# Kernel optimization log

Hardware: AMD Instinct MI355X
Metric: run time of the kernel (lower is better)

The kernel has to match this reference:

```python
import jax, jax.numpy as jnp
import numpy as np


def setup_inputs() -> dict:
    key = jax.random.key(0)
    k1, k2 = jax.random.split(key)
    B, N, M, D = 4, 8192, 8192, 3
    pred_points = jax.random.normal(k1, (B, N, D), dtype=jnp.float32)
    gt_points = jax.random.normal(k2, (B, M, D), dtype=jnp.float32)
    return {"pred_points": pred_points, "gt_points": gt_points}


def reference(pred_points, gt_points):
    p2 = jnp.sum(pred_points * pred_points, axis=-1)  # [B, N]
    g2 = jnp.sum(gt_points * gt_points, axis=-1)      # [B, M]
    cross = jnp.einsum("bnd,bmd->bnm", pred_points, gt_points)  # [B, N, M]
    d2 = p2[:, :, None] + g2[:, None, :] - 2.0 * cross
    dist = jnp.sqrt(jnp.maximum(d2, 0.0))             # [B, N, M]
    min_pred_to_gt = jnp.min(dist, axis=-1)           # [B, N]
    min_gt_to_pred = jnp.min(dist, axis=-2)           # [B, M]
    return min_pred_to_gt.mean() + min_gt_to_pred.mean()
```

## Files before the change

kernel.cpp:

```cpp
#include <hip/hip_runtime.h>


#define B_ 4
#define N_ 8192
#define TM 1024
#define SM (N_ / TM)
#define THREADS 512
#define INF32 3.4e38f

__device__ __forceinline__ float min3f(float a, float b, float c) {
  float d;
  asm("v_min3_f32 %0, %1, %2, %3" : "=v"(d) : "v"(a), "v"(b), "v"(c));
  return d;
}

__global__ __launch_bounds__(THREADS, 4) void chamfer_sym(
    const float* __restrict__ pred, const float* __restrict__ gt,
    float* __restrict__ rowpart, unsigned* __restrict__ colpart,
    float* __restrict__ accws, int RC) {
  __shared__ float4 mlds[TM];
  __shared__ unsigned colbuf[TM];

  const int b = blockIdx.z, tn = blockIdx.y, tm = blockIdx.x;
  const int tid = threadIdx.x;
  const int j = tid & 31;
  const int iq = tid >> 5;
  const int SN = gridDim.y;
  const int TN = N_ / SN;

  if (b == 0 && tn == 0 && tm == 0 && tid == 0) {
    accws[0] = 0.0f;
    ((unsigned*)accws)[1] = 0u;
  }

  const float* qsrc = pred + (size_t)b * N_ * 3;
  const float* tsrc = gt + (size_t)b * N_ * 3;

  if (tid < 256) {
    const float* tb = tsrc + (size_t)tm * TM * 3 + tid * 12;
    const float4 f0 = *(const float4*)(tb);
    const float4 f1 = *(const float4*)(tb + 4);
    const float4 f2 = *(const float4*)(tb + 8);
    float4 P0 = make_float4(f0.x, f0.y, f0.z, fmaf(f0.x,f0.x, fmaf(f0.y,f0.y, f0.z*f0.z)));
    float4 P1 = make_float4(f0.w, f1.x, f1.y, fmaf(f0.w,f0.w, fmaf(f1.x,f1.x, f1.y*f1.y)));
    float4 P2 = make_float4(f1.z, f1.w, f2.x, fmaf(f1.z,f1.z, fmaf(f1.w,f1.w, f2.x*f2.x)));
    float4 P3 = make_float4(f2.y, f2.z, f2.w, fmaf(f2.y,f2.y, fmaf(f2.z,f2.z, f2.w*f2.w)));
    const int s = (tid >> 3) & 3;
    const int base = tid * 4;
    mlds[base + (0 ^ s)] = P0;
    mlds[base + (1 ^ s)] = P1;
    mlds[base + (2 ^ s)] = P2;
    mlds[base + (3 ^ s)] = P3;
    ((uint4*)colbuf)[tid] = make_uint4(0x7F7FFFFFu, 0x7F7FFFFFu, 0x7F7FFFFFu, 0x7F7FFFFFu);
  }

  float colacc[32];
#pragma unroll
  for (int c = 0; c < 32; ++c) colacc[c] = INF32;

  __syncthreads();

  const int sw = (j >> 3) & 3;
  const int a0 = 4 * j + (0 ^ sw);
  const int a1 = 4 * j + (1 ^ sw);
  const int a2 = 4 * j + (2 ^ sw);
  const int a3 = 4 * j + (3 ^ sw);

  for (int rc = 0; rc < RC; ++rc) {
    const int r0 = tn * TN + rc * 64 + iq * 4;
    const float* qb = qsrc + (size_t)r0 * 3;
    const float4 g0 = *(const float4*)(qb);
    const float4 g1 = *(const float4*)(qb + 4);
    const float4 g2 = *(const float4*)(qb + 8);
    const float qx[4] = {g0.x, g0.w, g1.z, g2.y};
    const float qy[4] = {g0.y, g1.x, g1.w, g2.z};
    const float qz[4] = {g0.z, g1.y, g2.x, g2.w};
    float nx[4], ny[4], nz[4], q2[4], racc[4];
#pragma unroll
    for (int r = 0; r < 4; ++r) {
      nx[r] = -2.0f * qx[r]; ny[r] = -2.0f * qy[r]; nz[r] = -2.0f * qz[r];
      q2[r] = fmaf(qx[r], qx[r], fmaf(qy[r], qy[r], qz[r] * qz[r]));
      racc[r] = INF32;
    }

#pragma unroll
    for (int cs = 0; cs < 8; ++cs) {
      const float4 t0 = mlds[cs * 128 + a0];
      const float4 t1 = mlds[cs * 128 + a1];
      const float4 t2 = mlds[cs * 128 + a2];
      const float4 t3 = mlds[cs * 128 + a3];
      float sc[4][4];
#pragma unroll
      for (int r = 0; r < 4; ++r) {
        sc[r][0] = fmaf(nx[r], t0.x, fmaf(ny[r], t0.y, fmaf(nz[r], t0.z, t0.w)));
        sc[r][1] = fmaf(nx[r], t1.x, fmaf(ny[r], t1.y, fmaf(nz[r], t1.z, t1.w)));
        sc[r][2] = fmaf(nx[r], t2.x, fmaf(ny[r], t2.y, fmaf(nz[r], t2.z, t2.w)));
        sc[r][3] = fmaf(nx[r], t3.x, fmaf(ny[r], t3.y, fmaf(nz[r], t3.z, t3.w)));
        racc[r] = min3f(racc[r], sc[r][0], sc[r][1]);
        racc[r] = min3f(racc[r], sc[r][2], sc[r][3]);
      }
#pragma unroll
      for (int c = 0; c < 4; ++c) {
        colacc[cs*4+c] = min3f(colacc[cs*4+c], sc[0][c] + q2[0], sc[1][c] + q2[1]);
        colacc[cs*4+c] = min3f(colacc[cs*4+c], sc[2][c] + q2[2], sc[3][c] + q2[3]);
      }
    }

#pragma unroll
    for (int m = 1; m <= 16; m <<= 1) {
#pragma unroll
      for (int r = 0; r < 4; ++r)
        racc[r] = fminf(racc[r], __shfl_xor(racc[r], m, 64));
    }
    if (j == 0) {
      float4 v = make_float4(racc[0] + q2[0], racc[1] + q2[1],
                             racc[2] + q2[2], racc[3] + q2[3]);
      *(float4*)&rowpart[((size_t)b * SM + tm) * N_ + r0] = v;
    }
  }

#pragma unroll
  for (int c = 0; c < 32; ++c)
    colacc[c] = fminf(colacc[c], __shfl_xor(colacc[c], 32, 64));
  if ((tid & 32) == 0) {
#pragma unroll
    for (int cs = 0; cs < 8; ++cs)
#pragma unroll
      for (int c = 0; c < 4; ++c)
        atomicMin(&colbuf[cs * 128 + 4 * j + c],
                  __float_as_uint(fmaxf(colacc[cs*4+c], 0.0f)));
  }
  __syncthreads();
  {
    unsigned* dst = colpart + ((size_t)b * SN + tn) * N_ + tm * TM;
    dst[tid] = colbuf[tid];
    dst[tid + 512] = colbuf[tid + 512];
  }
}

__global__ __launch_bounds__(256) void chamfer_fin(
    const float* __restrict__ rowpart, const unsigned* __restrict__ colpart,
    float* __restrict__ accws, float* __restrict__ out, int SN) {
  const int t = blockIdx.x * 256 + threadIdx.x;
  float v;
  if (t < 32768) {
    const int b = t >> 13, n = t & (N_ - 1);
    const float* p = rowpart + (size_t)b * SM * N_ + n;
    v = p[0];
#pragma unroll
    for (int s2 = 1; s2 < SM; ++s2) v = fminf(v, p[(size_t)s2 * N_]);
  } else {
    const int u = t - 32768;
    const int b = u >> 13, n = u & (N_ - 1);
    const unsigned* p = colpart + (size_t)b * SN * N_ + n;
    unsigned m = p[0];
    for (int s2 = 1; s2 < SN; ++s2) m = min(m, p[(size_t)s2 * N_]);
    v = __uint_as_float(m);
  }
  float sum = sqrtf(fmaxf(v, 0.0f));
#pragma unroll
  for (int off = 32; off > 0; off >>= 1) sum += __shfl_down(sum, off, 64);
  __shared__ float ws4[4];
  const int lane = threadIdx.x & 63, wid = threadIdx.x >> 6;
  if (lane == 0) ws4[wid] = sum;
  __syncthreads();
  if (threadIdx.x == 0) {
    const float bs = (ws4[0] + ws4[1]) + (ws4[2] + ws4[3]);
    atomicAdd(&accws[0], bs);
    __threadfence();
    const unsigned old = atomicAdd(((unsigned*)accws) + 1, 1u);
    if (old == gridDim.x - 1) {
      __threadfence();
      const float tot = atomicAdd(&accws[0], 0.0f);
      out[0] = tot * (1.0f / 32768.0f);
    }
  }
}

extern "C" void kernel_launch(void* const* d_in, const int* in_sizes, int n_in,
                              void* d_out, int out_size, void* d_ws, size_t ws_size,
                              hipStream_t stream) {
  const float* pred = (const float*)d_in[0];
  const float* gt   = (const float*)d_in[1];
  float* out = (float*)d_out;

  float* accws = (float*)d_ws;
  float* rowpart = (float*)((char*)d_ws + 64);
  unsigned* colpart = (unsigned*)(rowpart + (size_t)B_ * SM * N_);

  const size_t base = 64 + (size_t)B_ * SM * N_ * 4;
  int RC = 16;
  if (ws_size >= base + (size_t)B_ * 32 * N_ * 4) RC = 4;
  else if (ws_size >= base + (size_t)B_ * 16 * N_ * 4) RC = 8;
  const int SN = N_ / (RC * 64);

  chamfer_sym<<<dim3(SM, SN, B_), THREADS, 0, stream>>>(
      pred, gt, rowpart, colpart, accws, RC);
  chamfer_fin<<<256, 256, 0, stream>>>(rowpart, colpart, accws, out, SN);
}
```

Measured before the change: 104.8 us.

## Use packed FP32 FMA with 8-row register tiles and global atomicMin reductions

The inner distance loop now uses v_pk_fma_f32/v_pk_add_f32 on pairs of query points, with an interleaved LDS layout (padded rows of 160) that stores x/y/z/|t|^2 pairs together. Each thread now handles 8 query rows per chunk instead of 4, and occupancy hint drops from 4 to 2. Per-tile partial row/column minima are replaced by global atomicMin into a single memset buffer, which shrinks the finalize kernel to one vector load per thread. This adds a memset launch and global atomic contention in exchange for fewer VALU ops per pair and less partial-result traffic.

```diff
diff --git a/kernel.cpp b/kernel.cpp
--- a/kernel.cpp
+++ b/kernel.cpp
@@ -4,118 +4,173 @@
 #define B_ 4
 #define N_ 8192
 #define TM 1024
-#define SM (N_ / TM)
+#define SM 8
+#define SN 16
+#define TN 512
 #define THREADS 512
-#define INF32 3.4e38f
+
+typedef float f32x2 __attribute__((ext_vector_type(2)));
+typedef float f32x4 __attribute__((ext_vector_type(4)));
 
 __device__ __forceinline__ float min3f(float a, float b, float c) {
   float d;
   asm("v_min3_f32 %0, %1, %2, %3" : "=v"(d) : "v"(a), "v"(b), "v"(c));
   return d;
 }
-
-__global__ __launch_bounds__(THREADS, 4) void chamfer_sym(
+__device__ __forceinline__ f32x2 mk2(float a, float b) { f32x2 r; r.x = a; r.y = b; return r; }
+
+__device__ __forceinline__ f32x2 pk_fma_blo(f32x2 bc, f32x2 b, f32x2 c) {
+  f32x2 d;
+  asm("v_pk_fma_f32 %0, %1, %2, %3 op_sel:[0,0,0] op_sel_hi:[0,1,1]"
+      : "=v"(d) : "v"(bc), "v"(b), "v"(c));
+  return d;
+}
+__device__ __forceinline__ f32x2 pk_fma_bhi(f32x2 bc, f32x2 b, f32x2 c) {
+  f32x2 d;
+  asm("v_pk_fma_f32 %0, %1, %2, %3 op_sel:[1,0,0] op_sel_hi:[1,1,1]"
+      : "=v"(d) : "v"(bc), "v"(b), "v"(c));
+  return d;
+}
+__device__ __forceinline__ f32x2 pk_add_blo(f32x2 a, f32x2 bc) {
+  f32x2 d;
+  asm("v_pk_add_f32 %0, %1, %2 op_sel:[0,0] op_sel_hi:[1,0]"
+      : "=v"(d) : "v"(a), "v"(bc));
+  return d;
+}
+__device__ __forceinline__ f32x2 pk_add_bhi(f32x2 a, f32x2 bc) {
+  f32x2 d;
+  asm("v_pk_add_f32 %0, %1, %2 op_sel:[0,1] op_sel_hi:[1,1]"
+      : "=v"(d) : "v"(a), "v"(bc));
+  return d;
+}
+
+__global__ __launch_bounds__(THREADS, 2) void chamfer_sym(
     const float* __restrict__ pred, const float* __restrict__ gt,
-    float* __restrict__ rowpart, unsigned* __restrict__ colpart,
-    float* __restrict__ accws, int RC) {
-  __shared__ float4 mlds[TM];
+    unsigned* __restrict__ rowmin, unsigned* __restrict__ colmin,
+    float* __restrict__ accws) {
+  __shared__ f32x4 mlds[8 * 160];
   __shared__ unsigned colbuf[TM];
 
-  const int b = blockIdx.z, tn = blockIdx.y, tm = blockIdx.x;
+  const int bb = blockIdx.z, tn = blockIdx.y, tm = blockIdx.x;
   const int tid = threadIdx.x;
   const int j = tid & 31;
   const int iq = tid >> 5;
-  const int SN = gridDim.y;
-  const int TN = N_ / SN;
-
-  if (b == 0 && tn == 0 && tm == 0 && tid == 0) {
-    accws[0] = 0.0f;
-    ((unsigned*)accws)[1] = 0u;
-  }
-
-  const float* qsrc = pred + (size_t)b * N_ * 3;
-  const float* tsrc = gt + (size_t)b * N_ * 3;
+
+  if (bb == 0 && tn == 0 && tm == 0 && tid < 2)
+    ((unsigned*)accws)[tid] = 0u;
+
+  const float* qsrc = pred + (size_t)bb * N_ * 3;
+  const float* tsrc = gt + (size_t)bb * N_ * 3;
 
   if (tid < 256) {
     const float* tb = tsrc + (size_t)tm * TM * 3 + tid * 12;
-    const float4 f0 = *(const float4*)(tb);
-    const float4 f1 = *(const float4*)(tb + 4);
-    const float4 f2 = *(const float4*)(tb + 8);
-    float4 P0 = make_float4(f0.x, f0.y, f0.z, fmaf(f0.x,f0.x, fmaf(f0.y,f0.y, f0.z*f0.z)));
-    float4 P1 = make_float4(f0.w, f1.x, f1.y, fmaf(f0.w,f0.w, fmaf(f1.x,f1.x, f1.y*f1.y)));
-    float4 P2 = make_float4(f1.z, f1.w, f2.x, fmaf(f1.z,f1.z, fmaf(f1.w,f1.w, f2.x*f2.x)));
-    float4 P3 = make_float4(f2.y, f2.z, f2.w, fmaf(f2.y,f2.y, fmaf(f2.z,f2.z, f2.w*f2.w)));
-    const int s = (tid >> 3) & 3;
-    const int base = tid * 4;
-    mlds[base + (0 ^ s)] = P0;
-    mlds[base + (1 ^ s)] = P1;
-    mlds[base + (2 ^ s)] = P2;
-    mlds[base + (3 ^ s)] = P3;
-    ((uint4*)colbuf)[tid] = make_uint4(0x7F7FFFFFu, 0x7F7FFFFFu, 0x7F7FFFFFu, 0x7F7FFFFFu);
+    const f32x4 f0 = *(const f32x4*)(tb);
+    const f32x4 f1 = *(const f32x4*)(tb + 4);
+    const f32x4 f2 = *(const f32x4*)(tb + 8);
+    const float x0 = f0.x, y0 = f0.y, z0 = f0.z;
+    const float x1 = f0.w, y1 = f1.x, z1 = f1.y;
+    const float x2 = f1.z, y2 = f1.w, z2 = f2.x;
+    const float x3 = f2.y, y3 = f2.z, z3 = f2.w;
+    const float w0 = fmaf(x0, x0, fmaf(y0, y0, z0 * z0));
+    const float w1 = fmaf(x1, x1, fmaf(y1, y1, z1 * z1));
+    const float w2 = fmaf(x2, x2, fmaf(y2, y2, z2 * z2));
+    const float w3 = fmaf(x3, x3, fmaf(y3, y3, z3 * z3));
+    const int base = (tid >> 5) * 160 + 5 * (tid & 31);
+    f32x4 A0; A0.x = x0; A0.y = x1; A0.z = y0; A0.w = y1;
+    f32x4 B0; B0.x = z0; B0.y = z1; B0.z = w0; B0.w = w1;
+    f32x4 A1; A1.x = x2; A1.y = x3; A1.z = y2; A1.w = y3;
+    f32x4 B1; B1.x = z2; B1.y = z3; B1.z = w2; B1.w = w3;
+    mlds[base + 0] = A0; mlds[base + 1] = B0;
+    mlds[base + 2] = A1; mlds[base + 3] = B1;
+    uint4 inf4; inf4.x = inf4.y = inf4.z = inf4.w = 0xFFFFFFFFu;
+    ((uint4*)colbuf)[tid] = inf4;
   }
 
   float colacc[32];
 #pragma unroll
-  for (int c = 0; c < 32; ++c) colacc[c] = INF32;
+  for (int c = 0; c < 32; ++c) colacc[c] = 3.4e38f;
 
   __syncthreads();
 
-  const int sw = (j >> 3) & 3;
-  const int a0 = 4 * j + (0 ^ sw);
-  const int a1 = 4 * j + (1 ^ sw);
-  const int a2 = 4 * j + (2 ^ sw);
-  const int a3 = 4 * j + (3 ^ sw);
-
-  for (int rc = 0; rc < RC; ++rc) {
-    const int r0 = tn * TN + rc * 64 + iq * 4;
+#define ROW(r, RR, SEL)                                                \
+  f32x2 d##r;                                                          \
+  {                                                                    \
+    f32x2 s = pk_fma_##SEL(nzp[RR], zz, ww);                           \
+    s = pk_fma_##SEL(nyp[RR], yy, s);                                  \
+    s = pk_fma_##SEL(nxp[RR], xx, s);                                  \
+    racc[r] = min3f(racc[r], s.x, s.y);                                \
+    d##r = pk_add_##SEL(s, q2p[RR]);                                   \
+  }
+
+#define PAIR(CIDX)                                                     \
+  {                                                                    \
+    ROW(0, 0, blo) ROW(1, 0, bhi) ROW(2, 1, blo) ROW(3, 1, bhi)        \
+    ROW(4, 2, blo) ROW(5, 2, bhi) ROW(6, 3, blo) ROW(7, 3, bhi)        \
+    colacc[CIDX] = min3f(colacc[CIDX], min3f(d0.x, d1.x, d2.x),        \
+                         min3f(d3.x, d4.x, d5.x));                     \
+    colacc[CIDX] = min3f(colacc[CIDX], d6.x, d7.x);                    \
+    colacc[CIDX + 1] = min3f(colacc[CIDX + 1], min3f(d0.y, d1.y, d2.y),\
+                             min3f(d3.y, d4.y, d5.y));                 \
+    colacc[CIDX + 1] = min3f(colacc[CIDX + 1], d6.y, d7.y);            \
+  }
+
+  for (int rc = 0; rc < 4; ++rc) {
+    const int r0 = tn * TN + rc * 128 + iq * 8;
     const float* qb = qsrc + (size_t)r0 * 3;
-    const float4 g0 = *(const float4*)(qb);
-    const float4 g1 = *(const float4*)(qb + 4);
-    const float4 g2 = *(const float4*)(qb + 8);
-    const float qx[4] = {g0.x, g0.w, g1.z, g2.y};
-    const float qy[4] = {g0.y, g1.x, g1.w, g2.z};
-    const float qz[4] = {g0.z, g1.y, g2.x, g2.w};
-    float nx[4], ny[4], nz[4], q2[4], racc[4];
-#pragma unroll
-    for (int r = 0; r < 4; ++r) {
-      nx[r] = -2.0f * qx[r]; ny[r] = -2.0f * qy[r]; nz[r] = -2.0f * qz[r];
-      q2[r] = fmaf(qx[r], qx[r], fmaf(qy[r], qy[r], qz[r] * qz[r]));
-      racc[r] = INF32;
-    }
+    const f32x4 a0 = *(const f32x4*)(qb);
+    const f32x4 a1 = *(const f32x4*)(qb + 4);
+    const f32x4 a2 = *(const f32x4*)(qb + 8);
+    const f32x4 a3 = *(const f32x4*)(qb + 12);
+    const f32x4 a4 = *(const f32x4*)(qb + 16);
+    const f32x4 a5 = *(const f32x4*)(qb + 20);
+    const float px[8] = {a0.x, a0.w, a1.z, a2.y, a3.x, a3.w, a4.z, a5.y};
+    const float py[8] = {a0.y, a1.x, a1.w, a2.z, a3.y, a4.x, a4.w, a5.z};
+    const float pz[8] = {a0.z, a1.y, a2.x, a2.w, a3.z, a4.y, a5.x, a5.w};
+    f32x2 nxp[4], nyp[4], nzp[4], q2p[4];
+#pragma unroll
+    for (int k = 0; k < 4; ++k) {
+      nxp[k] = mk2(-2.f * px[2 * k], -2.f * px[2 * k + 1]);
+      nyp[k] = mk2(-2.f * py[2 * k], -2.f * py[2 * k + 1]);
+      nzp[k] = mk2(-2.f * pz[2 * k], -2.f * pz[2 * k + 1]);
+      q2p[k] = mk2(
+          fmaf(px[2*k], px[2*k], fmaf(py[2*k], py[2*k], pz[2*k] * pz[2*k])),
+          fmaf(px[2*k+1], px[2*k+1],
+               fmaf(py[2*k+1], py[2*k+1], pz[2*k+1] * pz[2*k+1])));
+    }
+
+    float racc[8];
+#pragma unroll
+    for (int r = 0; r < 8; ++r) racc[r] = 3.4e38f;
 
 #pragma unroll
     for (int cs = 0; cs < 8; ++cs) {
-      const float4 t0 = mlds[cs * 128 + a0];
-      const float4 t1 = mlds[cs * 128 + a1];
-      const float4 t2 = mlds[cs * 128 + a2];
-      const float4 t3 = mlds[cs * 128 + a3];
-      float sc[4][4];
-#pragma unroll
-      for (int r = 0; r < 4; ++r) {
-        sc[r][0] = fmaf(nx[r], t0.x, fmaf(ny[r], t0.y, fmaf(nz[r], t0.z, t0.w)));
-        sc[r][1] = fmaf(nx[r], t1.x, fmaf(ny[r], t1.y, fmaf(nz[r], t1.z, t1.w)));
-        sc[r][2] = fmaf(nx[r], t2.x, fmaf(ny[r], t2.y, fmaf(nz[r], t2.z, t2.w)));
-        sc[r][3] = fmaf(nx[r], t3.x, fmaf(ny[r], t3.y, fmaf(nz[r], t3.z, t3.w)));
-        racc[r] = min3f(racc[r], sc[r][0], sc[r][1]);
-        racc[r] = min3f(racc[r], sc[r][2], sc[r][3]);
+      const int base = cs * 160 + 5 * j;
+      const f32x4 e0 = mlds[base + 0];
+      const f32x4 e1 = mlds[base + 1];
+      const f32x4 e2 = mlds[base + 2];
+      const f32x4 e3 = mlds[base + 3];
+      {
+        const f32x2 xx = e0.xy, yy = e0.zw, zz = e1.xy, ww = e1.zw;
+        PAIR(cs * 4)
       }
-#pragma unroll
-      for (int c = 0; c < 4; ++c) {
-        colacc[cs*4+c] = min3f(colacc[cs*4+c], sc[0][c] + q2[0], sc[1][c] + q2[1]);
-        colacc[cs*4+c] = min3f(colacc[cs*4+c], sc[2][c] + q2[2], sc[3][c] + q2[3]);
+      {
+        const f32x2 xx = e2.xy, yy = e2.zw, zz = e3.xy, ww = e3.zw;
+        PAIR(cs * 4 + 2)
       }
     }
 
 #pragma unroll
-    for (int m = 1; m <= 16; m <<= 1) {
-#pragma unroll
-      for (int r = 0; r < 4; ++r)
+    for (int m = 1; m <= 16; m <<= 1)
+#pragma unroll
+      for (int r = 0; r < 8; ++r)
         racc[r] = fminf(racc[r], __shfl_xor(racc[r], m, 64));
-    }
     if (j == 0) {
-      float4 v = make_float4(racc[0] + q2[0], racc[1] + q2[1],
-                             racc[2] + q2[2], racc[3] + q2[3]);
-      *(float4*)&rowpart[((size_t)b * SM + tm) * N_ + r0] = v;
+      unsigned* rp = rowmin + (size_t)bb * N_ + r0;
+#pragma unroll
+      for (int r = 0; r < 8; ++r) {
+        const float q2s = (r & 1) ? q2p[r >> 1].y : q2p[r >> 1].x;
+        atomicMin(&rp[r], __float_as_uint(fmaxf(racc[r] + q2s, 0.f)));
+      }
     }
   }
 
@@ -126,38 +181,27 @@
 #pragma unroll
     for (int cs = 0; cs < 8; ++cs)
 #pragma unroll
-      for (int c = 0; c < 4; ++c)
-        atomicMin(&colbuf[cs * 128 + 4 * j + c],
-                  __float_as_uint(fmaxf(colacc[cs*4+c], 0.0f)));
+      for (int k = 0; k < 4; ++k)
+        atomicMin(&colbuf[cs * 128 + 4 * j + k],
+                  __float_as_uint(fmaxf(colacc[cs * 4 + k], 0.f)));
   }
   __syncthreads();
   {
-    unsigned* dst = colpart + ((size_t)b * SN + tn) * N_ + tm * TM;
-    dst[tid] = colbuf[tid];
-    dst[tid + 512] = colbuf[tid + 512];
-  }
+    unsigned* cp = colmin + (size_t)bb * N_ + tm * TM;
+    atomicMin(&cp[tid], colbuf[tid]);
+    atomicMin(&cp[tid + 512], colbuf[tid + 512]);
+  }
+#undef ROW
+#undef PAIR
 }
 
 __global__ __launch_bounds__(256) void chamfer_fin(
-    const float* __restrict__ rowpart, const unsigned* __restrict__ colpart,
-    float* __restrict__ accws, float* __restrict__ out, int SN) {
+    const unsigned* __restrict__ minbuf, float* __restrict__ accws,
+    float* __restrict__ out) {
   const int t = blockIdx.x * 256 + threadIdx.x;
-  float v;
-  if (t < 32768) {
-    const int b = t >> 13, n = t & (N_ - 1);
-    const float* p = rowpart + (size_t)b * SM * N_ + n;
-    v = p[0];
-#pragma unroll
-    for (int s2 = 1; s2 < SM; ++s2) v = fminf(v, p[(size_t)s2 * N_]);
-  } else {
-    const int u = t - 32768;
-    const int b = u >> 13, n = u & (N_ - 1);
-    const unsigned* p = colpart + (size_t)b * SN * N_ + n;
-    unsigned m = p[0];
-    for (int s2 = 1; s2 < SN; ++s2) m = min(m, p[(size_t)s2 * N_]);
-    v = __uint_as_float(m);
-  }
-  float sum = sqrtf(fmaxf(v, 0.0f));
+  const uint4 v = ((const uint4*)minbuf)[t];
+  float sum = sqrtf(__uint_as_float(v.x)) + sqrtf(__uint_as_float(v.y)) +
+              sqrtf(__uint_as_float(v.z)) + sqrtf(__uint_as_float(v.w));
 #pragma unroll
   for (int off = 32; off > 0; off >>= 1) sum += __shfl_down(sum, off, 64);
   __shared__ float ws4[4];
@@ -185,16 +229,11 @@
   float* out = (float*)d_out;
 
   float* accws = (float*)d_ws;
-  float* rowpart = (float*)((char*)d_ws + 64);
-  unsigned* colpart = (unsigned*)(rowpart + (size_t)B_ * SM * N_);
-
-  const size_t base = 64 + (size_t)B_ * SM * N_ * 4;
-  int RC = 16;
-  if (ws_size >= base + (size_t)B_ * 32 * N_ * 4) RC = 4;
-  else if (ws_size >= base + (size_t)B_ * 16 * N_ * 4) RC = 8;
-  const int SN = N_ / (RC * 64);
-
+  unsigned* rowmin = (unsigned*)((char*)d_ws + 64);
+  unsigned* colmin = rowmin + (size_t)B_ * N_;
+
+  hipMemsetAsync(rowmin, 0xFF, (size_t)2 * B_ * N_ * sizeof(unsigned), stream);
   chamfer_sym<<<dim3(SM, SN, B_), THREADS, 0, stream>>>(
-      pred, gt, rowpart, colpart, accws, RC);
-  chamfer_fin<<<256, 256, 0, stream>>>(rowpart, colpart, accws, out, SN);
-}
+      pred, gt, rowmin, colmin, accws);
+  chamfer_fin<<<64, 256, 0, stream>>>(rowmin, accws, out);
+}
```

Measured after the change: 101.5 us. 3.2% less time.
